# Kernel optimization log

Hardware: AMD Instinct MI355X
Metric: run time of the kernel (lower is better)

## Reference

```python
import jax, jax.numpy as jnp
import numpy as np

B, N, S, P, D = 128, 4096, 32, 64, 128  # batch, wafers, stages, PMs, embed dim
NORM = 300.0


def gather(src, idx):
    # src: [B, n, D], idx: [B, m] int -> [B, m, D]
    return jnp.take_along_axis(src, idx[:, :, None], axis=1)


def setup_inputs() -> dict:
    key = jax.random.key(0)
    ks = jax.random.split(key, 16)
    return {
        "encoded_row": jax.random.normal(ks[0], (B, N, D), jnp.float32),
        "encoded_col": jax.random.normal(ks[1], (B, S, D), jnp.float32),
        "clock": jax.random.uniform(ks[2], (B, 1), jnp.float32) * NORM,
        "loc_process_end_time": jax.random.uniform(ks[3], (B, P), jnp.float32) * (2.0 * NORM),
        "W_dyn": jax.random.normal(ks[4], (2, D), jnp.float32) * 0.05,
        "W_concat": jax.random.normal(ks[5], (3 * D, D), jnp.float32) * 0.05,
        "W_robot": jax.random.normal(ks[6], (3 * D, D), jnp.float32) * 0.05,
        "loc_hold_wafer": jax.random.randint(ks[7], (B, P), 0, N),
        "loc_stage": jax.random.randint(ks[8], (B, P), 1, S + 1),
        "robot_arm1_loc": jax.random.randint(ks[9], (B, 1), 0, P + 2),
        "robot_arm2_loc": jax.random.randint(ks[10], (B, 1), 0, P + 2),
        "arm1_recipe": jax.random.randint(ks[11], (B, 1), 0, N),
        "arm2_recipe": jax.random.randint(ks[12], (B, 1), 0, N),
        "arm1_next_stage": jax.random.randint(ks[13], (B, 1), 0, S + 2),
        "arm2_next_stage": jax.random.randint(ks[14], (B, 1), 0, S + 2),
    }


def reference(encoded_row, encoded_col, clock, loc_process_end_time,
              W_dyn, W_concat, W_robot,
              loc_hold_wafer, loc_stage, robot_arm1_loc, robot_arm2_loc,
              arm1_recipe, arm2_recipe, arm1_next_stage, arm2_next_stage):
    dt = encoded_row.dtype
    # ---- get_PM_embedding ----
    clk = jnp.broadcast_to(clock, (B, P))
    remain_prs = jnp.where(loc_process_end_time > clk,
                           loc_process_end_time - clk, 0.0) / NORM
    remain_purge = jnp.zeros_like(remain_prs)
    pm_dyn = jnp.stack([remain_prs, remain_purge], axis=-1) @ W_dyn  # [B,P,D]

    rows_dummy = jnp.concatenate(
        [encoded_row, jnp.zeros((B, 1, D), dt)], axis=1)          # [B,N+1,D]
    lot_idx = jnp.where(loc_hold_wafer >= 0, loc_hold_wafer, N)
    pm_wafer = gather(rows_dummy, lot_idx)                         # [B,P,D]
    pm_stage = gather(encoded_col, loc_stage - 1)                  # [B,P,D]
    pm_emb = jnp.concatenate([pm_stage, pm_wafer, pm_dyn], -1) @ W_concat

    # ---- get_robot_embedding ----
    loc_emb = jnp.concatenate(
        [jnp.zeros((B, 1, D), dt), pm_emb, jnp.ones((B, 1, D), dt)], axis=1)
    cols_pad = jnp.concatenate(
        [jnp.zeros((B, 1, D), dt), encoded_col, jnp.zeros((B, 1, D), dt)], axis=1)

    def arm_embed(loc_idx, recipe, next_stage):
        a_loc = gather(loc_emb, loc_idx)                           # [B,1,D]
        a_wafer = gather(rows_dummy, jnp.where(recipe >= 0, recipe, N))
        a_ns = gather(cols_pad, jnp.where(next_stage >= 0, next_stage, 0))
        return jnp.concatenate([a_loc, a_wafer, a_ns], -1) @ W_robot

    arm1 = arm_embed(robot_arm1_loc, arm1_recipe, arm1_next_stage)
    arm2 = arm_embed(robot_arm2_loc, arm2_recipe, arm2_next_stage)

    return jnp.concatenate([pm_emb, arm1, arm2], axis=1)           # [B,P+2,D]
```

## Files before the change

### kernel.cpp

```cpp
#include <hip/hip_runtime.h>
#include <stdint.h>

namespace {
constexpr int B = 128;
constexpr int N = 4096;
constexpr int S = 32;
constexpr int P = 64;
constexpr int D = 128;
constexpr int K = 384;
constexpr int KS = K / 32;
constexpr int ROWPAD = 196;
constexpr int PM_BLOCKS = (B * P) / 16;
constexpr int ARM_BLOCKS = (2 * B) / 16;
}

typedef __attribute__((ext_vector_type(8))) short short8;
typedef __attribute__((ext_vector_type(4))) float f32x4;

__device__ __forceinline__ uint32_t f2bf(float f) {
    union { float f; uint32_t u; } v; v.f = f;
    return (v.u + 0x7FFFu + ((v.u >> 16) & 1u)) >> 16;
}
__device__ __forceinline__ uint32_t pack2(float x, float y) {
    return f2bf(x) | (f2bf(y) << 16);
}

__global__ __launch_bounds__(256) void prep_w_kernel(
    const float* __restrict__ Wc, const float* __restrict__ Wr,
    uint32_t* __restrict__ Wsw)
{
    const int idx = blockIdx.x * 256 + threadIdx.x;
    const bool is_c = (idx < 6144);
    const float* W = is_c ? Wc : Wr;
    const int l = is_c ? idx : (idx - 6144);
    const int n  = l & 15;
    const int t  = (l >> 4) & 7;
    const int q  = (l >> 7) & 3;
    const int ks = l >> 9;
    const int col  = t * 16 + n;
    const int krow = ks * 32 + q * 8;
    uint32_t pk[4];
    #pragma unroll
    for (int jj = 0; jj < 4; ++jj) {
        const float a = W[(size_t)(krow + 2 * jj) * D + col];
        const float b = W[(size_t)(krow + 2 * jj + 1) * D + col];
        pk[jj] = pack2(a, b);
    }
    ((uint4*)Wsw)[idx] = make_uint4(pk[0], pk[1], pk[2], pk[3]);
}

__global__ __launch_bounds__(256) void fused_kernel(
    const float* __restrict__ enc_row,
    const float* __restrict__ enc_col,
    const float* __restrict__ clockp,
    const float* __restrict__ lpet,
    const float* __restrict__ W_dyn,
    const int*   __restrict__ lhw,
    const int*   __restrict__ lstage,
    const int* __restrict__ loc1, const int* __restrict__ loc2,
    const int* __restrict__ rec1, const int* __restrict__ rec2,
    const int* __restrict__ nst1, const int* __restrict__ nst2,
    const uint32_t* __restrict__ Wsw,
    float* __restrict__ out)
{
    __shared__ uint32_t xs[16 * ROWPAD];
    __shared__ uint32_t xs2[16 * ROWPAD];
    __shared__ int locs[16];

    const int lane = threadIdx.x & 63;
    const int wave = threadIdx.x >> 6;
    const int q = lane >> 4;
    const int n16 = lane & 15;
    const int t0 = wave * 2, t1 = t0 + 1;
    const short8* wswc = (const short8*)Wsw;
    const short8* wswr = wswc + 6144;
    const float2 wd = ((const float2*)W_dyn)[lane];

    if (blockIdx.x < PM_BLOCKS) {
        const int r0 = blockIdx.x * 16;
        #pragma unroll
        for (int rr = 0; rr < 4; ++rr) {
            const int r = wave * 4 + rr;
            const int rid = r0 + r;
            const int b = rid >> 6;
            const float c = clockp[b];
            const float tt = lpet[rid];
            const float rem = (tt > c) ? (tt - c) * (1.0f / 300.0f) : 0.0f;
            const int wi = lhw[rid];
            const int cs = lstage[rid] - 1;
            const float2 sv = ((const float2*)(enc_col + ((size_t)b * S + cs) * D))[lane];
            float2 wv = make_float2(0.f, 0.f);
            if (wi >= 0)
                wv = ((const float2*)(enc_row + ((size_t)b * N + wi) * D))[lane];
            xs[r * ROWPAD + 0 * 64 + lane] = pack2(sv.x, sv.y);
            xs[r * ROWPAD + 1 * 64 + lane] = pack2(wv.x, wv.y);
            xs[r * ROWPAD + 2 * 64 + lane] = pack2(wd.x * rem, wd.y * rem);
        }
        __syncthreads();

        f32x4 acc0 = {0.f, 0.f, 0.f, 0.f};
        f32x4 acc1 = {0.f, 0.f, 0.f, 0.f};
        #pragma unroll
        for (int ks = 0; ks < KS; ++ks) {
            const short8 a = *(const short8*)(xs + n16 * ROWPAD + ks * 16 + q * 4);
            const short8 b0 = wswc[((ks * 4 + q) * 8 + t0) * 16 + n16];
            const short8 b1 = wswc[((ks * 4 + q) * 8 + t1) * 16 + n16];
            acc0 = __builtin_amdgcn_mfma_f32_16x16x32_bf16(a, b0, acc0, 0, 0, 0);
            acc1 = __builtin_amdgcn_mfma_f32_16x16x32_bf16(a, b1, acc1, 0, 0, 0);
        }
        #pragma unroll
        for (int i = 0; i < 4; ++i) {
            const int row = q * 4 + i;
            const int rid = r0 + row;
            const int bb = rid >> 6;
            const int pp = rid & 63;
            float* o = out + ((size_t)bb * (P + 2) + pp) * D;
            o[t0 * 16 + n16] = acc0[i];
            o[t1 * 16 + n16] = acc1[i];
        }
    } else {
        const int ab = blockIdx.x - PM_BLOCKS;
        #pragma unroll
        for (int rr = 0; rr < 4; ++rr) {
            const int r = wave * 4 + rr;
            const int aid = ab * 16 + r;
            const int b = aid >> 1;
            const int arm = aid & 1;
            const int loc = arm ? loc2[b] : loc1[b];
            const int rec = arm ? rec2[b] : rec1[b];
            int ns = arm ? nst2[b] : nst1[b];
            if (ns < 0) ns = 0;
            if (lane == 0) locs[r] = loc;

            if (loc >= 1 && loc <= P) {
                const int rid = b * P + (loc - 1);
                const float c = clockp[b];
                const float tt = lpet[rid];
                const float rem = (tt > c) ? (tt - c) * (1.0f / 300.0f) : 0.0f;
                const int wi = lhw[rid];
                const int cs = lstage[rid] - 1;
                const float2 sv = ((const float2*)(enc_col + ((size_t)b * S + cs) * D))[lane];
                float2 wv = make_float2(0.f, 0.f);
                if (wi >= 0)
                    wv = ((const float2*)(enc_row + ((size_t)b * N + wi) * D))[lane];
                xs[r * ROWPAD + 0 * 64 + lane] = pack2(sv.x, sv.y);
                xs[r * ROWPAD + 1 * 64 + lane] = pack2(wv.x, wv.y);
                xs[r * ROWPAD + 2 * 64 + lane] = pack2(wd.x * rem, wd.y * rem);
            } else {
                xs[r * ROWPAD + 0 * 64 + lane] = 0u;
                xs[r * ROWPAD + 1 * 64 + lane] = 0u;
                xs[r * ROWPAD + 2 * 64 + lane] = 0u;
            }

            float2 awv = make_float2(0.f, 0.f);
            if (rec >= 0)
                awv = ((const float2*)(enc_row + ((size_t)b * N + rec) * D))[lane];
            float2 anv = make_float2(0.f, 0.f);
            if (ns >= 1 && ns <= S)
                anv = ((const float2*)(enc_col + ((size_t)b * S + (ns - 1)) * D))[lane];
            xs2[r * ROWPAD + 1 * 64 + lane] = pack2(awv.x, awv.y);
            xs2[r * ROWPAD + 2 * 64 + lane] = pack2(anv.x, anv.y);
        }
        __syncthreads();

        f32x4 acc0 = {0.f, 0.f, 0.f, 0.f};
        f32x4 acc1 = {0.f, 0.f, 0.f, 0.f};
        #pragma unroll
        for (int ks = 0; ks < KS; ++ks) {
            const short8 a = *(const short8*)(xs + n16 * ROWPAD + ks * 16 + q * 4);
            const short8 b0 = wswc[((ks * 4 + q) * 8 + t0) * 16 + n16];
            const short8 b1 = wswc[((ks * 4 + q) * 8 + t1) * 16 + n16];
            acc0 = __builtin_amdgcn_mfma_f32_16x16x32_bf16(a, b0, acc0, 0, 0, 0);
            acc1 = __builtin_amdgcn_mfma_f32_16x16x32_bf16(a, b1, acc1, 0, 0, 0);
        }

        unsigned short* u2 = (unsigned short*)xs2;
        #pragma unroll
        for (int i = 0; i < 4; ++i) {
            const int row = q * 4 + i;
            const int lc = locs[row];
            float v0 = acc0[i], v1 = acc1[i];
            if (lc == 0)      { v0 = 0.f; v1 = 0.f; }
            if (lc == P + 1)  { v0 = 1.f; v1 = 1.f; }
            u2[row * (2 * ROWPAD) + t0 * 16 + n16] = (unsigned short)f2bf(v0);
            u2[row * (2 * ROWPAD) + t1 * 16 + n16] = (unsigned short)f2bf(v1);
        }
        __syncthreads();

        f32x4 racc0 = {0.f, 0.f, 0.f, 0.f};
        f32x4 racc1 = {0.f, 0.f, 0.f, 0.f};
        #pragma unroll
        for (int ks = 0; ks < KS; ++ks) {
            const short8 a = *(const short8*)(xs2 + n16 * ROWPAD + ks * 16 + q * 4);
            const short8 b0 = wswr[((ks * 4 + q) * 8 + t0) * 16 + n16];
            const short8 b1 = wswr[((ks * 4 + q) * 8 + t1) * 16 + n16];
            racc0 = __builtin_amdgcn_mfma_f32_16x16x32_bf16(a, b0, racc0, 0, 0, 0);
            racc1 = __builtin_amdgcn_mfma_f32_16x16x32_bf16(a, b1, racc1, 0, 0, 0);
        }
        #pragma unroll
        for (int i = 0; i < 4; ++i) {
            const int row = q * 4 + i;
            const int aid = ab * 16 + row;
            const int bb = aid >> 1;
            const int arm = aid & 1;
            float* o = out + ((size_t)bb * (P + 2) + P + arm) * D;
            o[t0 * 16 + n16] = racc0[i];
            o[t1 * 16 + n16] = racc1[i];
        }
    }
}

extern "C" void kernel_launch(void* const* d_in, const int* in_sizes, int n_in,
                              void* d_out, int out_size, void* d_ws, size_t ws_size,
                              hipStream_t stream) {
    const float* enc_row  = (const float*)d_in[0];
    const float* enc_col  = (const float*)d_in[1];
    const float* clockp   = (const float*)d_in[2];
    const float* lpet     = (const float*)d_in[3];
    const float* W_dyn    = (const float*)d_in[4];
    const float* W_concat = (const float*)d_in[5];
    const float* W_robot  = (const float*)d_in[6];
    const int*   lhw      = (const int*)d_in[7];
    const int*   lstage   = (const int*)d_in[8];
    const int*   loc1     = (const int*)d_in[9];
    const int*   loc2     = (const int*)d_in[10];
    const int*   rec1     = (const int*)d_in[11];
    const int*   rec2     = (const int*)d_in[12];
    const int*   nst1     = (const int*)d_in[13];
    const int*   nst2     = (const int*)d_in[14];
    float* out = (float*)d_out;
    uint32_t* Wsw = (uint32_t*)d_ws;

    prep_w_kernel<<<48, 256, 0, stream>>>(W_concat, W_robot, Wsw);
    fused_kernel<<<PM_BLOCKS + ARM_BLOCKS, 256, 0, stream>>>(
        enc_row, enc_col, clockp, lpet, W_dyn, lhw, lstage,
        loc1, loc2, rec1, rec2, nst1, nst2, Wsw, out);
}
```

Before: 330.4 us.

## Drop weight prep kernel, convert weights inline, and double PM rows per block

Removes the separate weight pre-swizzle/bf16 conversion kernel launch; each block now reads fp32 W_concat/W_robot directly and converts fragments to bf16 in registers. PM blocks process 32 rows instead of 16, reusing each loaded B fragment across two M tiles so the per-block weight conversion is amortized. This trades an extra launch for redundant strided fp32 weight loads and conversion in every block, and halves the number of PM blocks.

```diff
diff --git a/kernel.cpp b/kernel.cpp
--- a/kernel.cpp
+++ b/kernel.cpp
@@ -1,4 +1,5 @@
 #include <hip/hip_runtime.h>
+#include <hip/hip_bf16.h>
 #include <stdint.h>
 
 namespace {
@@ -10,7 +11,7 @@
 constexpr int K = 384;
 constexpr int KS = K / 32;
 constexpr int ROWPAD = 196;
-constexpr int PM_BLOCKS = (B * P) / 16;
+constexpr int PM_BLOCKS = (B * P) / 32;
 constexpr int ARM_BLOCKS = (2 * B) / 16;
 }
 
@@ -22,31 +23,19 @@
     return (v.u + 0x7FFFu + ((v.u >> 16) & 1u)) >> 16;
 }
 __device__ __forceinline__ uint32_t pack2(float x, float y) {
-    return f2bf(x) | (f2bf(y) << 16);
-}
-
-__global__ __launch_bounds__(256) void prep_w_kernel(
-    const float* __restrict__ Wc, const float* __restrict__ Wr,
-    uint32_t* __restrict__ Wsw)
-{
-    const int idx = blockIdx.x * 256 + threadIdx.x;
-    const bool is_c = (idx < 6144);
-    const float* W = is_c ? Wc : Wr;
-    const int l = is_c ? idx : (idx - 6144);
-    const int n  = l & 15;
-    const int t  = (l >> 4) & 7;
-    const int q  = (l >> 7) & 3;
-    const int ks = l >> 9;
-    const int col  = t * 16 + n;
-    const int krow = ks * 32 + q * 8;
-    uint32_t pk[4];
+    union { __hip_bfloat162 h; uint32_t u; } cv;
+    cv.h = __float22bfloat162_rn(make_float2(x, y));
+    return cv.u;
+}
+
+__device__ __forceinline__ short8 load_bfrag(const float* __restrict__ W,
+                                             int ks, int q, int col) {
+    const float* p = W + (size_t)((ks * 32 + q * 8) * D + col);
+    union { uint32_t u[4]; short8 s; } cv;
     #pragma unroll
-    for (int jj = 0; jj < 4; ++jj) {
-        const float a = W[(size_t)(krow + 2 * jj) * D + col];
-        const float b = W[(size_t)(krow + 2 * jj + 1) * D + col];
-        pk[jj] = pack2(a, b);
-    }
-    ((uint4*)Wsw)[idx] = make_uint4(pk[0], pk[1], pk[2], pk[3]);
+    for (int jj = 0; jj < 4; ++jj)
+        cv.u[jj] = pack2(p[(2 * jj) * D], p[(2 * jj + 1) * D]);
+    return cv.s;
 }
 
 __global__ __launch_bounds__(256) void fused_kernel(
@@ -55,16 +44,16 @@
     const float* __restrict__ clockp,
     const float* __restrict__ lpet,
     const float* __restrict__ W_dyn,
+    const float* __restrict__ Wc,
+    const float* __restrict__ Wr,
     const int*   __restrict__ lhw,
     const int*   __restrict__ lstage,
     const int* __restrict__ loc1, const int* __restrict__ loc2,
     const int* __restrict__ rec1, const int* __restrict__ rec2,
     const int* __restrict__ nst1, const int* __restrict__ nst2,
-    const uint32_t* __restrict__ Wsw,
     float* __restrict__ out)
 {
-    __shared__ uint32_t xs[16 * ROWPAD];
-    __shared__ uint32_t xs2[16 * ROWPAD];
+    __shared__ uint32_t xs[32 * ROWPAD];
     __shared__ int locs[16];
 
     const int lane = threadIdx.x & 63;
@@ -72,15 +61,13 @@
     const int q = lane >> 4;
     const int n16 = lane & 15;
     const int t0 = wave * 2, t1 = t0 + 1;
-    const short8* wswc = (const short8*)Wsw;
-    const short8* wswr = wswc + 6144;
     const float2 wd = ((const float2*)W_dyn)[lane];
 
     if (blockIdx.x < PM_BLOCKS) {
-        const int r0 = blockIdx.x * 16;
-        #pragma unroll
-        for (int rr = 0; rr < 4; ++rr) {
-            const int r = wave * 4 + rr;
+        const int r0 = blockIdx.x * 32;
+        #pragma unroll
+        for (int rr = 0; rr < 8; ++rr) {
+            const int r = wave * 8 + rr;
             const int rid = r0 + r;
             const int b = rid >> 6;
             const float c = clockp[b];
@@ -98,28 +85,37 @@
         }
         __syncthreads();
 
-        f32x4 acc0 = {0.f, 0.f, 0.f, 0.f};
-        f32x4 acc1 = {0.f, 0.f, 0.f, 0.f};
+        f32x4 acc00 = {0.f, 0.f, 0.f, 0.f};
+        f32x4 acc01 = {0.f, 0.f, 0.f, 0.f};
+        f32x4 acc10 = {0.f, 0.f, 0.f, 0.f};
+        f32x4 acc11 = {0.f, 0.f, 0.f, 0.f};
         #pragma unroll
         for (int ks = 0; ks < KS; ++ks) {
-            const short8 a = *(const short8*)(xs + n16 * ROWPAD + ks * 16 + q * 4);
-            const short8 b0 = wswc[((ks * 4 + q) * 8 + t0) * 16 + n16];
-            const short8 b1 = wswc[((ks * 4 + q) * 8 + t1) * 16 + n16];
-            acc0 = __builtin_amdgcn_mfma_f32_16x16x32_bf16(a, b0, acc0, 0, 0, 0);
-            acc1 = __builtin_amdgcn_mfma_f32_16x16x32_bf16(a, b1, acc1, 0, 0, 0);
+            const short8 a0 = *(const short8*)(xs + n16 * ROWPAD + ks * 16 + q * 4);
+            const short8 a1 = *(const short8*)(xs + (16 + n16) * ROWPAD + ks * 16 + q * 4);
+            const short8 b0 = load_bfrag(Wc, ks, q, t0 * 16 + n16);
+            const short8 b1 = load_bfrag(Wc, ks, q, t1 * 16 + n16);
+            acc00 = __builtin_amdgcn_mfma_f32_16x16x32_bf16(a0, b0, acc00, 0, 0, 0);
+            acc01 = __builtin_amdgcn_mfma_f32_16x16x32_bf16(a0, b1, acc01, 0, 0, 0);
+            acc10 = __builtin_amdgcn_mfma_f32_16x16x32_bf16(a1, b0, acc10, 0, 0, 0);
+            acc11 = __builtin_amdgcn_mfma_f32_16x16x32_bf16(a1, b1, acc11, 0, 0, 0);
         }
         #pragma unroll
         for (int i = 0; i < 4; ++i) {
-            const int row = q * 4 + i;
-            const int rid = r0 + row;
-            const int bb = rid >> 6;
-            const int pp = rid & 63;
-            float* o = out + ((size_t)bb * (P + 2) + pp) * D;
-            o[t0 * 16 + n16] = acc0[i];
-            o[t1 * 16 + n16] = acc1[i];
+            #pragma unroll
+            for (int mt = 0; mt < 2; ++mt) {
+                const int row = mt * 16 + q * 4 + i;
+                const int rid = r0 + row;
+                const int bb = rid >> 6;
+                const int pp = rid & 63;
+                float* o = out + ((size_t)bb * (P + 2) + pp) * D;
+                o[t0 * 16 + n16] = mt ? acc10[i] : acc00[i];
+                o[t1 * 16 + n16] = mt ? acc11[i] : acc01[i];
+            }
         }
     } else {
         const int ab = blockIdx.x - PM_BLOCKS;
+        uint32_t* xs2 = xs + 16 * ROWPAD;
         #pragma unroll
         for (int rr = 0; rr < 4; ++rr) {
             const int r = wave * 4 + rr;
@@ -168,8 +164,8 @@
         #pragma unroll
         for (int ks = 0; ks < KS; ++ks) {
             const short8 a = *(const short8*)(xs + n16 * ROWPAD + ks * 16 + q * 4);
-            const short8 b0 = wswc[((ks * 4 + q) * 8 + t0) * 16 + n16];
-            const short8 b1 = wswc[((ks * 4 + q) * 8 + t1) * 16 + n16];
+            const short8 b0 = load_bfrag(Wc, ks, q, t0 * 16 + n16);
+            const short8 b1 = load_bfrag(Wc, ks, q, t1 * 16 + n16);
             acc0 = __builtin_amdgcn_mfma_f32_16x16x32_bf16(a, b0, acc0, 0, 0, 0);
             acc1 = __builtin_amdgcn_mfma_f32_16x16x32_bf16(a, b1, acc1, 0, 0, 0);
         }
@@ -192,8 +188,8 @@
         #pragma unroll
         for (int ks = 0; ks < KS; ++ks) {
             const short8 a = *(const short8*)(xs2 + n16 * ROWPAD + ks * 16 + q * 4);
-            const short8 b0 = wswr[((ks * 4 + q) * 8 + t0) * 16 + n16];
-            const short8 b1 = wswr[((ks * 4 + q) * 8 + t1) * 16 + n16];
+            const short8 b0 = load_bfrag(Wr, ks, q, t0 * 16 + n16);
+            const short8 b1 = load_bfrag(Wr, ks, q, t1 * 16 + n16);
             racc0 = __builtin_amdgcn_mfma_f32_16x16x32_bf16(a, b0, racc0, 0, 0, 0);
             racc1 = __builtin_amdgcn_mfma_f32_16x16x32_bf16(a, b1, racc1, 0, 0, 0);
         }
@@ -229,10 +225,9 @@
     const int*   nst1     = (const int*)d_in[13];
     const int*   nst2     = (const int*)d_in[14];
     float* out = (float*)d_out;
-    uint32_t* Wsw = (uint32_t*)d_ws;
-
-    prep_w_kernel<<<48, 256, 0, stream>>>(W_concat, W_robot, Wsw);
+    (void)d_ws; (void)ws_size;
+
     fused_kernel<<<PM_BLOCKS + ARM_BLOCKS, 256, 0, stream>>>(
-        enc_row, enc_col, clockp, lpet, W_dyn, lhw, lstage,
-        loc1, loc2, rec1, rec2, nst1, nst2, Wsw, out);
-}
+        enc_row, enc_col, clockp, lpet, W_dyn, W_concat, W_robot, lhw, lstage,
+        loc1, loc2, rec1, rec2, nst1, nst2, out);
+}
```

Result: no change. 331.7 us (+0.4%).
